# Kernel tuning notes

Hardware: AMD Instinct MI355X
Metric: run time of the kernel (lower is better)

Reference implementation:

```python
import jax, jax.numpy as jnp
import numpy as np

S, B, E, H, DFF = 1024, 4, 1024, 16, 4096
D = E // H  # head_dim = 64
EPS = 1e-5


def setup_inputs() -> dict:
    key = jax.random.key(0)
    ks = jax.random.split(key, 16)
    rn = lambda k, shape, s: jax.random.normal(k, shape, jnp.float32) * s
    # RoPE tables (half-rotation), theta=10000
    inv_freq = 1.0 / (10000.0 ** (jnp.arange(0, D, 2, dtype=jnp.float32) / D))  # [D/2]
    ang = jnp.arange(S, dtype=jnp.float32)[:, None] * inv_freq[None, :]          # [S, D/2]
    return {
        "q": rn(ks[0], (S, B, E), 1.0),
        "in_proj_w": rn(ks[1], (3 * E, E), E ** -0.5),
        "in_proj_b": rn(ks[2], (3 * E,), 0.02),
        "out_w": rn(ks[3], (E, E), E ** -0.5),
        "out_b": rn(ks[4], (E,), 0.02),
        "ln1_g": jnp.ones((E,), jnp.float32) + rn(ks[5], (E,), 0.02),
        "ln1_b": rn(ks[6], (E,), 0.02),
        "ln2_g": jnp.ones((E,), jnp.float32) + rn(ks[7], (E,), 0.02),
        "ln2_b": rn(ks[8], (E,), 0.02),
        "ff1_w": rn(ks[9], (DFF, E), E ** -0.5),
        "ff1_b": rn(ks[10], (DFF,), 0.02),
        "ff2_w": rn(ks[11], (E, DFF), DFF ** -0.5),
        "ff2_b": rn(ks[12], (E,), 0.02),
        "rope_cos": jnp.cos(ang),
        "rope_sin": jnp.sin(ang),
    }


def _layernorm(x, g, b):
    mu = jnp.mean(x, -1, keepdims=True)
    var = jnp.mean((x - mu) ** 2, -1, keepdims=True)
    return (x - mu) * jax.lax.rsqrt(var + EPS) * g + b


def reference(q, in_proj_w, in_proj_b, out_w, out_b, ln1_g, ln1_b, ln2_g, ln2_b,
              ff1_w, ff1_b, ff2_w, ff2_b, rope_cos, rope_sin):
    s, b, e = q.shape
    d = 2 * rope_cos.shape[-1]
    h = e // d
    # pre-norm (self-attention: k = v = q, so norm computed once)
    xq = _layernorm(q, ln1_g, ln1_b)
    # fused QKV projection
    qkv = xq @ in_proj_w.T + in_proj_b            # [s, b, 3e]
    qh, kh, vh = jnp.split(qkv, 3, axis=-1)
    qh = qh.reshape(s, b, h, d)
    kh = kh.reshape(s, b, h, d)
    vh = vh.reshape(s, b, h, d)

    def rope(t):
        t1, t2 = jnp.split(t, 2, axis=-1)          # [s, b, h, d/2] each
        c = rope_cos[:, None, None, :]
        sn = rope_sin[:, None, None, :]
        return jnp.concatenate([t1 * c - t2 * sn, t1 * sn + t2 * c], axis=-1)

    qh = rope(qh)
    kh = rope(kh)
    # attention (ssmax='none' -> identity scaling, dropout=0, no masks)
    scores = jnp.einsum("sbhd,tbhd->bhst", qh, kh) / jnp.sqrt(jnp.float32(d))
    attn = jax.nn.softmax(scores, axis=-1)
    ao = jnp.einsum("bhst,tbhd->sbhd", attn, vh).reshape(s, b, e)
    ao = ao @ out_w.T + out_b
    # residual + pre-norm FFN
    x = q + ao
    y = _layernorm(x, ln2_g, ln2_b)
    ff = jax.nn.gelu(y @ ff1_w.T + ff1_b, approximate=False) @ ff2_w.T + ff2_b
    return x + ff
```

## Files before the change

kernel.cpp:

```cpp
#include <hip/hip_runtime.h>
#include <hip/hip_bf16.h>
#include <stdint.h>

typedef float f32x4 __attribute__((ext_vector_type(4)));
typedef __bf16 bf16x8 __attribute__((ext_vector_type(8)));

__device__ __forceinline__ unsigned short f2bf(float f) {
    union { float f; unsigned u; } v; v.f = f;
    unsigned r = v.u + 0x7fffu + ((v.u >> 16) & 1u);
    return (unsigned short)(r >> 16);
}
__device__ __forceinline__ float bf2f(unsigned short u) {
    union { unsigned u; float f; } v; v.u = ((unsigned)u) << 16;
    return v.f;
}
__device__ __forceinline__ unsigned cvt_pk_bf16(float lo, float hi) {
    unsigned r;
    asm("v_cvt_pk_bf16_f32 %0, %1, %2" : "=v"(r) : "v"(lo), "v"(hi));
    return r;
}

__device__ __forceinline__ void gl_lds16(const void* g, void* l) {
    __builtin_amdgcn_global_load_lds(
        (const __attribute__((address_space(1))) void*)(unsigned long long)(uintptr_t)g,
        (__attribute__((address_space(3))) void*)(unsigned)(uintptr_t)l,
        16, 0, 0);
}

__global__ __launch_bounds__(256) void cvt_kernel(const float* __restrict__ in,
                                                  unsigned short* __restrict__ outp) {
    int i = blockIdx.x * 256 + threadIdx.x;
    float4 v = ((const float4*)in)[i];
    ushort4 o;
    o.x = f2bf(v.x); o.y = f2bf(v.y); o.z = f2bf(v.z); o.w = f2bf(v.w);
    ((ushort4*)outp)[i] = o;
}

__global__ __launch_bounds__(256) void ln_kernel(const float* __restrict__ x,
                                                 const float* __restrict__ g,
                                                 const float* __restrict__ b,
                                                 unsigned short* __restrict__ outp) {
    const int row = blockIdx.x;
    const int t = threadIdx.x;
    const float4 v = ((const float4*)(x + (size_t)row * 1024))[t];
    float s = v.x + v.y + v.z + v.w;
    float s2 = v.x * v.x + v.y * v.y + v.z * v.z + v.w * v.w;
    #pragma unroll
    for (int off = 1; off < 64; off <<= 1) {
        s  += __shfl_xor(s, off);
        s2 += __shfl_xor(s2, off);
    }
    __shared__ float red[8];
    const int w = t >> 6;
    if ((t & 63) == 0) { red[w * 2] = s; red[w * 2 + 1] = s2; }
    __syncthreads();
    s  = red[0] + red[2] + red[4] + red[6];
    s2 = red[1] + red[3] + red[5] + red[7];
    const float mu = s * (1.0f / 1024.0f);
    const float var = s2 * (1.0f / 1024.0f) - mu * mu;
    const float rstd = rsqrtf(var + 1e-5f);
    const float4 gv = ((const float4*)g)[t];
    const float4 bv = ((const float4*)b)[t];
    ushort4 o;
    o.x = f2bf((v.x - mu) * rstd * gv.x + bv.x);
    o.y = f2bf((v.y - mu) * rstd * gv.y + bv.y);
    o.z = f2bf((v.z - mu) * rstd * gv.z + bv.z);
    o.w = f2bf((v.w - mu) * rstd * gv.w + bv.w);
    ((ushort4*)(outp + (size_t)row * 1024))[t] = o;
}

__global__ __launch_bounds__(512) void rope_kernel(const unsigned short* __restrict__ qkv,
                                                   const float* __restrict__ rc,
                                                   const float* __restrict__ rs,
                                                   unsigned short* __restrict__ Qr,
                                                   unsigned short* __restrict__ Kr) {
    const int sb = blockIdx.x;
    const int s = sb >> 2, b = sb & 3;
    const int t = threadIdx.x;
    const int h = t >> 5, d = t & 31;
    const size_t rowo = (size_t)sb * 3072;
    const float c = rc[s * 32 + d];
    const float sn = rs[s * 32 + d];
    const size_t ho = ((size_t)(b * 16 + h) * 1024 + s) * 64;

    const float q1 = bf2f(qkv[rowo + h * 64 + d]);
    const float q2 = bf2f(qkv[rowo + h * 64 + d + 32]);
    Qr[ho + d]      = f2bf((q1 * c - q2 * sn) * 0.125f);
    Qr[ho + d + 32] = f2bf((q1 * sn + q2 * c) * 0.125f);

    const float k1 = bf2f(qkv[rowo + 1024 + h * 64 + d]);
    const float k2 = bf2f(qkv[rowo + 1024 + h * 64 + d + 32]);
    Kr[ho + d]      = f2bf(k1 * c - k2 * sn);
    Kr[ho + d + 32] = f2bf(k1 * sn + k2 * c);
}

__global__ __launch_bounds__(256) void vt_kernel(const unsigned short* __restrict__ qkv,
                                                 unsigned short* __restrict__ Vt) {
    __shared__ unsigned short t[64][66];
    const int s0 = blockIdx.x * 64;
    const int bh = blockIdx.y;
    const int b = bh >> 4, h = bh & 15;
    const int tid = threadIdx.x;
    const int si = tid >> 3, c = (tid & 7) * 8;
    #pragma unroll
    for (int r = 0; r < 2; r++) {
        const int s = si + r * 32;
        union { uint4 u; unsigned short sh[8]; } v;
        v.u = *(const uint4*)&qkv[((size_t)(s0 + s) * 4 + b) * 3072 + 2048 + h * 64 + c];
        #pragma unroll
        for (int i = 0; i < 8; i++) t[c + i][s] = v.sh[i];
    }
    __syncthreads();
    #pragma unroll
    for (int r = 0; r < 2; r++) {
        const int d = si + r * 32;
        const unsigned* rp = (const unsigned*)((const char*)&t[0][0] + d * 132 + c * 2);
        uint4 ov;
        ov.x = rp[0]; ov.y = rp[1]; ov.z = rp[2]; ov.w = rp[3];
        *(uint4*)&Vt[((size_t)bh * 64 + d) * 1024 + s0 + c] = ov;
    }
}

template <int EPI, int BM, int BN, int WM, int WN, bool CM>
__global__ __launch_bounds__((BM / WM) * (BN / WN) * 64, 2)
void gemm4(const unsigned short* __restrict__ A, const unsigned short* __restrict__ Bw,
           const float* __restrict__ bias, const float* __restrict__ res,
           void* __restrict__ Cout, int N, int K, int nbx) {
    constexpr int WAVES_N = BN / WN;
    constexpr int THREADS = (BM / WM) * (BN / WN) * 64;
    constexpr int MR = WM / 16, NR = WN / 16;
    constexpr int ASZ = BM * 64, BSZ = BN * 64;
    constexpr int RPP = THREADS / 8;
    static_assert(BM / RPP + BN / RPP == 8, "STAGE must issue exactly 8 loads");
    __shared__ __attribute__((aligned(16))) unsigned short As[2 * ASZ];
    __shared__ __attribute__((aligned(16))) unsigned short Bs[2 * BSZ];

    const int nwg = gridDim.x;
    const int swz = (blockIdx.x & 7) * (nwg >> 3) + (blockIdx.x >> 3);
    const int nby = nwg / nbx;
    const int bx = CM ? (swz / nby) : (swz % nbx);
    const int by = CM ? (swz % nby) : (swz / nbx);
    const int bm = by * BM, bn = bx * BN;

    const int tid = threadIdx.x;
    const int w = tid >> 6, l = tid & 63;
    const int wr = w / WAVES_N, wc = w % WAVES_N;
    const int lm = l & 15, lg = l >> 4, lx = lm & 7;

    const int srow = tid >> 3;
    const int sgx = ((tid & 7) ^ (srow & 7)) * 8;
    const unsigned short* Ag = A + (size_t)(bm + srow) * K + sgx;
    const unsigned short* Bg = Bw + (size_t)(bn + srow) * K + sgx;

    const int c0 = ((lg ^ lx) << 3);
    const int c1 = (((4 + lg) ^ lx) << 3);

    f32x4 acc[MR][NR];
    #pragma unroll
    for (int i = 0; i < MR; i++)
        #pragma unroll
        for (int j = 0; j < NR; j++) acc[i][j] = f32x4{0.f, 0.f, 0.f, 0.f};

    auto STAGE = [&](int buf, int k0) {
        #pragma unroll
        for (int i = 0; i < BM / RPP; i++)
            gl_lds16(Ag + (size_t)i * RPP * K + k0, &As[buf * ASZ + i * RPP * 64 + tid * 8]);
        #pragma unroll
        for (int i = 0; i < BN / RPP; i++)
            gl_lds16(Bg + (size_t)i * RPP * K + k0, &Bs[buf * BSZ + i * RPP * 64 + tid * 8]);
    };

    const int NT = K >> 6;
    STAGE(0, 0);
    STAGE(1, 64);

    int cur = 0;
    for (int t = 0; t < NT; ++t) {
        if (t + 1 < NT) asm volatile("s_waitcnt vmcnt(8)" ::: "memory");
        else            asm volatile("s_waitcnt vmcnt(0)" ::: "memory");
        __builtin_amdgcn_s_barrier();
        asm volatile("" ::: "memory");

        const int ab = cur * ASZ, bb = cur * BSZ;
        #pragma unroll
        for (int h = 0; h < 2; h++) {
            const int cc = h ? c1 : c0;
            bf16x8 af[MR], bfr[NR];
            #pragma unroll
            for (int mi = 0; mi < MR; mi++)
                af[mi] = *(const bf16x8*)&As[ab + (wr * WM + mi * 16 + lm) * 64 + cc];
            #pragma unroll
            for (int ni = 0; ni < NR; ni++)
                bfr[ni] = *(const bf16x8*)&Bs[bb + (wc * WN + ni * 16 + lm) * 64 + cc];
            __builtin_amdgcn_s_setprio(1);
            #pragma unroll
            for (int mi = 0; mi < MR; mi++)
                #pragma unroll
                for (int ni = 0; ni < NR; ni++)
                    acc[mi][ni] = __builtin_amdgcn_mfma_f32_16x16x32_bf16(
                        af[mi], bfr[ni], acc[mi][ni], 0, 0, 0);
            __builtin_amdgcn_s_setprio(0);
        }

        asm volatile("" ::: "memory");
        __builtin_amdgcn_s_barrier();
        asm volatile("" ::: "memory");
        if (t + 2 < NT) STAGE(cur, (t + 2) << 6);
        cur ^= 1;
    }

    const int r0 = bm + wr * WM + lg * 4;
    #pragma unroll
    for (int ni = 0; ni < NR; ni++) {
        const int col = bn + wc * WN + ni * 16 + lm;
        const float bc = bias[col];
        #pragma unroll
        for (int mi = 0; mi < MR; mi++) {
            #pragma unroll
            for (int j = 0; j < 4; j++) {
                const int row = r0 + mi * 16 + j;
                const size_t idx = (size_t)row * N + col;
                const float v = acc[mi][ni][j] + bc;
                if constexpr (EPI == 0) {
                    ((unsigned short*)Cout)[idx] = f2bf(v);
                } else if constexpr (EPI == 1) {
                    ((float*)Cout)[idx] = v + res[idx];
                } else if constexpr (EPI == 2) {
                    const float ge = 0.5f * v * (1.0f + erff(v * 0.70710678118654752f));
                    ((unsigned short*)Cout)[idx] = f2bf(ge);
                } else {
                    ((float*)Cout)[idx] = v + res[idx];
                }
            }
        }
    }
}

__global__ __launch_bounds__(256, 4)
void attn_kernel(const unsigned short* __restrict__ Qr, const unsigned short* __restrict__ Kr,
                 const unsigned short* __restrict__ Vt, unsigned short* __restrict__ AO) {
    __shared__ __attribute__((aligned(16))) unsigned short Ks[64][72];
    __shared__ __attribute__((aligned(16))) unsigned short Vs[64][72];
    const int tid = threadIdx.x;
    const int w = tid >> 6, l = tid & 63;
    const int lm = l & 15, lg = l >> 4;
    const int qt = blockIdx.x, bh = blockIdx.y;
    const size_t hoff = (size_t)bh * (1024 * 64);

    const size_t qrow = hoff + (size_t)(qt * 64 + w * 16 + lm) * 64;
    const bf16x8 qf0 = *(const bf16x8*)&Qr[qrow + lg * 8];
    const bf16x8 qf1 = *(const bf16x8*)&Qr[qrow + 32 + lg * 8];

    float m = -1e30f, lsum = 0.f;
    f32x4 acc[4];
    #pragma unroll
    for (int i = 0; i < 4; i++) acc[i] = f32x4{0.f, 0.f, 0.f, 0.f};

    const int sr = tid >> 3, scc = (tid & 7) * 8;
    const int srcA = lm + 16 * ((2 * lg) & 3);
    const int srcB = lm + 16 * ((2 * lg + 1) & 3);
    const bool hi2 = (lg & 2) != 0;

    uint4 kr0 = *(const uint4*)&Kr[hoff + (size_t)sr * 64 + scc];
    uint4 kr1 = *(const uint4*)&Kr[hoff + (size_t)(sr + 32) * 64 + scc];
    uint4 vr0 = *(const uint4*)&Vt[hoff + (size_t)sr * 1024 + scc];
    uint4 vr1 = *(const uint4*)&Vt[hoff + (size_t)(sr + 32) * 1024 + scc];

    for (int kt = 0; kt < 16; kt++) {
        __syncthreads();
        *(uint4*)&Ks[sr][scc]      = kr0;
        *(uint4*)&Ks[sr + 32][scc] = kr1;
        *(uint4*)&Vs[sr][scc]      = vr0;
        *(uint4*)&Vs[sr + 32][scc] = vr1;
        __syncthreads();
        if (kt < 15) {
            const size_t kb = hoff + (size_t)(kt + 1) * 64 * 64;
            kr0 = *(const uint4*)&Kr[kb + (size_t)sr * 64 + scc];
            kr1 = *(const uint4*)&Kr[kb + (size_t)(sr + 32) * 64 + scc];
            vr0 = *(const uint4*)&Vt[hoff + (size_t)sr * 1024 + (kt + 1) * 64 + scc];
            vr1 = *(const uint4*)&Vt[hoff + (size_t)(sr + 32) * 1024 + (kt + 1) * 64 + scc];
        }

        f32x4 st[4];
        #pragma unroll
        for (int nt = 0; nt < 4; nt++) {
            const bf16x8 kf0 = *(const bf16x8*)&Ks[nt * 16 + lm][lg * 8];
            const bf16x8 kf1 = *(const bf16x8*)&Ks[nt * 16 + lm][32 + lg * 8];
            f32x4 s = f32x4{0.f, 0.f, 0.f, 0.f};
            s = __builtin_amdgcn_mfma_f32_16x16x32_bf16(kf0, qf0, s, 0, 0, 0);
            s = __builtin_amdgcn_mfma_f32_16x16x32_bf16(kf1, qf1, s, 0, 0, 0);
            st[nt] = s;
        }

        float tmax = st[0][0];
        #pragma unroll
        for (int nt = 0; nt < 4; nt++)
            #pragma unroll
            for (int j = 0; j < 4; j++) tmax = fmaxf(tmax, st[nt][j]);
        tmax = fmaxf(tmax, __shfl_xor(tmax, 16));
        tmax = fmaxf(tmax, __shfl_xor(tmax, 32));

        const float mnew = fmaxf(m, tmax);
        const float fac = __builtin_amdgcn_exp2f((m - mnew) * 1.4426950408889634f);
        m = mnew;

        unsigned pd[4][2];
        float rsum = 0.f;
        #pragma unroll
        for (int nt = 0; nt < 4; nt++) {
            const float p0 = __builtin_amdgcn_exp2f((st[nt][0] - mnew) * 1.4426950408889634f);
            const float p1 = __builtin_amdgcn_exp2f((st[nt][1] - mnew) * 1.4426950408889634f);
            const float p2 = __builtin_amdgcn_exp2f((st[nt][2] - mnew) * 1.4426950408889634f);
            const float p3 = __builtin_amdgcn_exp2f((st[nt][3] - mnew) * 1.4426950408889634f);
            rsum += (p0 + p1) + (p2 + p3);
            pd[nt][0] = cvt_pk_bf16(p0, p1);
            pd[nt][1] = cvt_pk_bf16(p2, p3);
        }
        rsum += __shfl_xor(rsum, 16);
        rsum += __shfl_xor(rsum, 32);
        lsum = lsum * fac + rsum;
        #pragma unroll
        for (int nt2 = 0; nt2 < 4; nt2++)
            #pragma unroll
            for (int j = 0; j < 4; j++) acc[nt2][j] *= fac;

        #pragma unroll
        for (int kt2 = 0; kt2 < 2; kt2++) {
            const int a0 = __shfl((int)pd[kt2 * 2][0], srcA);
            const int a1 = __shfl((int)pd[kt2 * 2 + 1][0], srcA);
            const int a2 = __shfl((int)pd[kt2 * 2][1], srcA);
            const int a3 = __shfl((int)pd[kt2 * 2 + 1][1], srcA);
            const int b0 = __shfl((int)pd[kt2 * 2][0], srcB);
            const int b1 = __shfl((int)pd[kt2 * 2 + 1][0], srcB);
            const int b2 = __shfl((int)pd[kt2 * 2][1], srcB);
            const int b3 = __shfl((int)pd[kt2 * 2 + 1][1], srcB);
            union { int u[4]; bf16x8 v; } pf;
            pf.u[0] = hi2 ? a1 : a0;
            pf.u[1] = hi2 ? a3 : a2;
            pf.u[2] = hi2 ? b1 : b0;
            pf.u[3] = hi2 ? b3 : b2;
            #pragma unroll
            for (int nt2 = 0; nt2 < 4; nt2++) {
                const bf16x8 vf = *(const bf16x8*)&Vs[nt2 * 16 + lm][kt2 * 32 + lg * 8];
                acc[nt2] = __builtin_amdgcn_mfma_f32_16x16x32_bf16(vf, pf.v, acc[nt2], 0, 0, 0);
            }
        }
    }

    const int b = bh >> 4, h = bh & 15;
    const float inv = 1.0f / lsum;
    const int s = qt * 64 + w * 16 + lm;
    #pragma unroll
    for (int nt2 = 0; nt2 < 4; nt2++) {
        ushort4 o;
        o.x = f2bf(acc[nt2][0] * inv);
        o.y = f2bf(acc[nt2][1] * inv);
        o.z = f2bf(acc[nt2][2] * inv);
        o.w = f2bf(acc[nt2][3] * inv);
        *(ushort4*)&AO[(size_t)(s * 4 + b) * 1024 + h * 64 + nt2 * 16 + lg * 4] = o;
    }
}

extern "C" void kernel_launch(void* const* d_in, const int* in_sizes, int n_in,
                              void* d_out, int out_size, void* d_ws, size_t ws_size,
                              hipStream_t stream) {
    const float* q    = (const float*)d_in[0];
    const float* w_in = (const float*)d_in[1];
    const float* b_in = (const float*)d_in[2];
    const float* w_o  = (const float*)d_in[3];
    const float* b_o  = (const float*)d_in[4];
    const float* g1   = (const float*)d_in[5];
    const float* be1  = (const float*)d_in[6];
    const float* g2   = (const float*)d_in[7];
    const float* be2  = (const float*)d_in[8];
    const float* w1   = (const float*)d_in[9];
    const float* b1   = (const float*)d_in[10];
    const float* w2   = (const float*)d_in[11];
    const float* b2   = (const float*)d_in[12];
    const float* rc   = (const float*)d_in[13];
    const float* rsn  = (const float*)d_in[14];
    float* outp = (float*)d_out;

    char* base = (char*)d_ws;
    if (ws_size < 109051904ull) return;

    unsigned short* wb_in  = (unsigned short*)(base + 0);
    unsigned short* wb_out = wb_in + 3145728;
    unsigned short* wb_ff1 = wb_out + 1048576;
    unsigned short* wb_ff2 = wb_ff1 + 4194304;
    unsigned short* xq  = (unsigned short*)(base + 25165824);
    unsigned short* qkv = (unsigned short*)(base + 33554432);
    unsigned short* hh  = (unsigned short*)(base + 33554432);
    unsigned short* Qr  = (unsigned short*)(base + 58720256);
    unsigned short* Kr  = (unsigned short*)(base + 67108864);
    unsigned short* Vt  = (unsigned short*)(base + 75497472);
    unsigned short* ao  = (unsigned short*)(base + 83886080);
    float*          x   = (float*)(base + 92274688);
    unsigned short* y   = xq;

    cvt_kernel<<<3072, 256, 0, stream>>>(w_in, wb_in);
    cvt_kernel<<<1024, 256, 0, stream>>>(w_o, wb_out);
    cvt_kernel<<<4096, 256, 0, stream>>>(w1, wb_ff1);
    cvt_kernel<<<4096, 256, 0, stream>>>(w2, wb_ff2);

    ln_kernel<<<4096, 256, 0, stream>>>(q, g1, be1, xq);
    gemm4<0, 128, 128, 64, 64, false><<<768, 256, 0, stream>>>(xq, wb_in, b_in, nullptr, qkv, 3072, 1024, 24);
    rope_kernel<<<4096, 512, 0, stream>>>(qkv, rc, rsn, Qr, Kr);
    vt_kernel<<<dim3(16, 64), 256, 0, stream>>>(qkv, Vt);
    attn_kernel<<<dim3(16, 64), 256, 0, stream>>>(Qr, Kr, Vt, ao);
    gemm4<1, 128, 128, 64, 64, true><<<256, 256, 0, stream>>>(ao, wb_out, b_o, q, x, 1024, 1024, 8);
    ln_kernel<<<4096, 256, 0, stream>>>(x, g2, be2, y);
    gemm4<2, 256, 256, 128, 64, false><<<256, 512, 0, stream>>>(y, wb_ff1, b1, nullptr, hh, 4096, 1024, 16);
    gemm4<3, 128, 128, 64, 64, true><<<256, 256, 0, stream>>>(hh, wb_ff2, b2, x, outp, 1024, 4096, 8);
}
```

Before: 233.9 us.

## Add 256x256 eight-wave GEMM with interleaved prefetch for QKV and FF1

Adds a dedicated 256x256-tile GEMM kernel with 8 waves that splits each K-step into four MFMA phases. Each phase interleaves one quarter of the next tile's global-to-LDS loads and raises wave priority around the MFMA blocks. The QKV projection moves from 768 128x128 tiles to 192 256x256 tiles, and FF1 moves from the generic template to the new kernel. QKV now launches fewer blocks than the device has CUs, which risks underfilling the GPU, and the extra barriers add sync cost in exchange for better overlap.

```diff
diff --git a/kernel.cpp b/kernel.cpp
--- a/kernel.cpp
+++ b/kernel.cpp
@@ -118,6 +118,152 @@
         uint4 ov;
         ov.x = rp[0]; ov.y = rp[1]; ov.z = rp[2]; ov.w = rp[3];
         *(uint4*)&Vt[((size_t)bh * 64 + d) * 1024 + s0 + c] = ov;
+    }
+}
+
+template <int EPI>
+__global__ __launch_bounds__(512, 2)
+void gemm8(const unsigned short* __restrict__ A, const unsigned short* __restrict__ Bw,
+           const float* __restrict__ bias, const float* __restrict__ res,
+           void* __restrict__ Cout, int N, int K, int nbx) {
+    constexpr int ASZ = 256 * 64;
+    __shared__ __attribute__((aligned(16))) unsigned short As[2 * ASZ];
+    __shared__ __attribute__((aligned(16))) unsigned short Bs[2 * ASZ];
+
+    const int nwg = gridDim.x;
+    const int swz = (blockIdx.x & 7) * (nwg >> 3) + (blockIdx.x >> 3);
+    const int bx = swz % nbx, by = swz / nbx;
+    const int bm = by * 256, bn = bx * 256;
+
+    const int tid = threadIdx.x;
+    const int w = tid >> 6, l = tid & 63;
+    const int wr = w >> 2, wc = w & 3;
+    const int lm = l & 15, lg = l >> 4, lx = lm & 7;
+
+    const int srow = tid >> 3;
+    const int sgx = ((tid & 7) ^ (srow & 7)) * 8;
+    const unsigned short* Ag = A + (size_t)(bm + srow) * K + sgx;
+    const unsigned short* Bg = Bw + (size_t)(bn + srow) * K + sgx;
+
+    const int c0 = ((lg ^ lx) << 3);
+    const int c1 = (((4 + lg) ^ lx) << 3);
+
+    f32x4 acc[8][4];
+    #pragma unroll
+    for (int i = 0; i < 8; i++)
+        #pragma unroll
+        for (int j = 0; j < 4; j++) acc[i][j] = f32x4{0.f, 0.f, 0.f, 0.f};
+
+    auto SP = [&](int buf, int k0, int p) {
+        gl_lds16(Ag + (size_t)(p * 64) * K + k0, &As[buf * ASZ + p * 4096 + tid * 8]);
+        gl_lds16(Bg + (size_t)(p * 64) * K + k0, &Bs[buf * ASZ + p * 4096 + tid * 8]);
+    };
+
+    SP(0, 0, 0); SP(0, 0, 1); SP(0, 0, 2); SP(0, 0, 3);
+
+    const int NT = K >> 6;
+    const int arow = wr * 128 + lm;
+    const int brow = wc * 64 + lm;
+    int cur = 0;
+
+    for (int t = 0; t < NT; ++t) {
+        const int ab = cur * ASZ, bb = cur * ASZ;
+        const int nk0 = (t + 1) << 6;
+        const bool pf = (t + 1 < NT);
+        bf16x8 bf0[4], bf1[4], af[4];
+
+        if (pf) {
+            SP(cur ^ 1, nk0, 0);
+            asm volatile("s_waitcnt vmcnt(2)" ::: "memory");
+        } else {
+            asm volatile("s_waitcnt vmcnt(0)" ::: "memory");
+        }
+        __builtin_amdgcn_s_barrier();
+        #pragma unroll
+        for (int ni = 0; ni < 4; ni++) {
+            bf0[ni] = *(const bf16x8*)&Bs[bb + (brow + ni * 16) * 64 + c0];
+            bf1[ni] = *(const bf16x8*)&Bs[bb + (brow + ni * 16) * 64 + c1];
+        }
+        #pragma unroll
+        for (int mi = 0; mi < 4; mi++)
+            af[mi] = *(const bf16x8*)&As[ab + (arow + mi * 16) * 64 + c0];
+        __builtin_amdgcn_s_barrier();
+        __builtin_amdgcn_s_setprio(1);
+        #pragma unroll
+        for (int mi = 0; mi < 4; mi++)
+            #pragma unroll
+            for (int ni = 0; ni < 4; ni++)
+                acc[mi][ni] = __builtin_amdgcn_mfma_f32_16x16x32_bf16(af[mi], bf0[ni], acc[mi][ni], 0, 0, 0);
+        __builtin_amdgcn_s_setprio(0);
+        __builtin_amdgcn_s_barrier();
+
+        if (pf) SP(cur ^ 1, nk0, 1);
+        #pragma unroll
+        for (int mi = 0; mi < 4; mi++)
+            af[mi] = *(const bf16x8*)&As[ab + (arow + mi * 16) * 64 + c1];
+        __builtin_amdgcn_s_barrier();
+        __builtin_amdgcn_s_setprio(1);
+        #pragma unroll
+        for (int mi = 0; mi < 4; mi++)
+            #pragma unroll
+            for (int ni = 0; ni < 4; ni++)
+                acc[mi][ni] = __builtin_amdgcn_mfma_f32_16x16x32_bf16(af[mi], bf1[ni], acc[mi][ni], 0, 0, 0);
+        __builtin_amdgcn_s_setprio(0);
+        __builtin_amdgcn_s_barrier();
+
+        if (pf) SP(cur ^ 1, nk0, 2);
+        #pragma unroll
+        for (int mi = 0; mi < 4; mi++)
+            af[mi] = *(const bf16x8*)&As[ab + (arow + 64 + mi * 16) * 64 + c0];
+        __builtin_amdgcn_s_barrier();
+        __builtin_amdgcn_s_setprio(1);
+        #pragma unroll
+        for (int mi = 0; mi < 4; mi++)
+            #pragma unroll
+            for (int ni = 0; ni < 4; ni++)
+                acc[mi + 4][ni] = __builtin_amdgcn_mfma_f32_16x16x32_bf16(af[mi], bf0[ni], acc[mi + 4][ni], 0, 0, 0);
+        __builtin_amdgcn_s_setprio(0);
+        __builtin_amdgcn_s_barrier();
+
+        if (pf) SP(cur ^ 1, nk0, 3);
+        #pragma unroll
+        for (int mi = 0; mi < 4; mi++)
+            af[mi] = *(const bf16x8*)&As[ab + (arow + 64 + mi * 16) * 64 + c1];
+        __builtin_amdgcn_s_barrier();
+        __builtin_amdgcn_s_setprio(1);
+        #pragma unroll
+        for (int mi = 0; mi < 4; mi++)
+            #pragma unroll
+            for (int ni = 0; ni < 4; ni++)
+                acc[mi + 4][ni] = __builtin_amdgcn_mfma_f32_16x16x32_bf16(af[mi], bf1[ni], acc[mi + 4][ni], 0, 0, 0);
+        __builtin_amdgcn_s_setprio(0);
+        __builtin_amdgcn_s_barrier();
+
+        cur ^= 1;
+    }
+
+    const int r0 = bm + wr * 128 + lg * 4;
+    #pragma unroll
+    for (int ni = 0; ni < 4; ni++) {
+        const int col = bn + wc * 64 + ni * 16 + lm;
+        const float bc = bias[col];
+        #pragma unroll
+        for (int mi = 0; mi < 8; mi++) {
+            #pragma unroll
+            for (int j = 0; j < 4; j++) {
+                const int row = r0 + mi * 16 + j;
+                const size_t idx = (size_t)row * N + col;
+                const float v = acc[mi][ni][j] + bc;
+                if constexpr (EPI == 0) {
+                    ((unsigned short*)Cout)[idx] = f2bf(v);
+                } else if constexpr (EPI == 2) {
+                    const float ge = 0.5f * v * (1.0f + erff(v * 0.70710678118654752f));
+                    ((unsigned short*)Cout)[idx] = f2bf(ge);
+                } else {
+                    ((float*)Cout)[idx] = v + res[idx];
+                }
+            }
+        }
     }
 }
 
@@ -404,12 +550,12 @@
     cvt_kernel<<<4096, 256, 0, stream>>>(w2, wb_ff2);
 
     ln_kernel<<<4096, 256, 0, stream>>>(q, g1, be1, xq);
-    gemm4<0, 128, 128, 64, 64, false><<<768, 256, 0, stream>>>(xq, wb_in, b_in, nullptr, qkv, 3072, 1024, 24);
+    gemm8<0><<<192, 512, 0, stream>>>(xq, wb_in, b_in, nullptr, qkv, 3072, 1024, 12);
     rope_kernel<<<4096, 512, 0, stream>>>(qkv, rc, rsn, Qr, Kr);
     vt_kernel<<<dim3(16, 64), 256, 0, stream>>>(qkv, Vt);
     attn_kernel<<<dim3(16, 64), 256, 0, stream>>>(Qr, Kr, Vt, ao);
     gemm4<1, 128, 128, 64, 64, true><<<256, 256, 0, stream>>>(ao, wb_out, b_o, q, x, 1024, 1024, 8);
     ln_kernel<<<4096, 256, 0, stream>>>(x, g2, be2, y);
-    gemm4<2, 256, 256, 128, 64, false><<<256, 512, 0, stream>>>(y, wb_ff1, b1, nullptr, hh, 4096, 1024, 16);
+    gemm8<2><<<256, 512, 0, stream>>>(y, wb_ff1, b1, nullptr, hh, 4096, 1024, 16);
     gemm4<3, 128, 128, 64, 64, true><<<256, 256, 0, stream>>>(hh, wb_ff2, b2, x, outp, 1024, 4096, 8);
 }
```

After: 240.9 us. 3.0% more time.

## Add single-buffered 256x128 GEMM kernel for QKV and FF1 projections

Applied to the files above, without the earlier changes.

Introduces a new gemmW kernel with 256x128 tiles, 8 waves of 128x32 each, and a single 64 KB LDS buffer, no double buffering. It is used for the QKV and FF1 GEMMs in place of gemm4. The epilogue stages bf16 results through LDS so global stores are coalesced 16-byte writes. The intent is higher occupancy (launch bounds 512,4) and wider per-wave MFMA reuse along M. The cost is that loads no longer overlap compute within a block, which may expose memory latency, and the launch-bounds target limits registers for the 16 accumulators.

```diff
diff --git a/kernel.cpp b/kernel.cpp
--- a/kernel.cpp
+++ b/kernel.cpp
@@ -118,6 +118,99 @@
         uint4 ov;
         ov.x = rp[0]; ov.y = rp[1]; ov.z = rp[2]; ov.w = rp[3];
         *(uint4*)&Vt[((size_t)bh * 64 + d) * 1024 + s0 + c] = ov;
+    }
+}
+
+template <int EPI>
+__global__ __launch_bounds__(512, 4)
+void gemmW(const unsigned short* __restrict__ A, const unsigned short* __restrict__ Bw,
+           const float* __restrict__ bias, unsigned short* __restrict__ Cout,
+           int N, int K, int nbx) {
+    __shared__ __attribute__((aligned(16))) unsigned short smem[32768];
+    unsigned short* As = smem;
+    unsigned short* Bs = smem + 16384;
+
+    const int nwg = gridDim.x;
+    const int swz = (blockIdx.x & 7) * (nwg >> 3) + (blockIdx.x >> 3);
+    const int by = swz / nbx, bx = swz % nbx;
+    const int bm = by * 256, bn = bx * 128;
+
+    const int tid = threadIdx.x;
+    const int w = tid >> 6, l = tid & 63;
+    const int wr = w >> 2, wc = w & 3;
+    const int lm = l & 15, lg = l >> 4, lx = lm & 7;
+
+    const int srow = tid >> 3;
+    const int sgx = ((tid & 7) ^ (srow & 7)) * 8;
+    const int sdst = (tid & 7) * 8;
+    const unsigned short* Ag = A + (size_t)(bm + srow) * K + sgx;
+    const unsigned short* Bg = Bw + (size_t)(bn + srow) * K + sgx;
+
+    const int c0 = ((lg ^ lx) << 3);
+    const int c1 = (((4 + lg) ^ lx) << 3);
+
+    f32x4 acc[8][2];
+    #pragma unroll
+    for (int i = 0; i < 8; i++)
+        #pragma unroll
+        for (int j = 0; j < 2; j++) acc[i][j] = f32x4{0.f, 0.f, 0.f, 0.f};
+
+    const int arow = wr * 128 + lm;
+    const int brow = wc * 32 + lm;
+
+    for (int k0 = 0; k0 < K; k0 += 64) {
+        __syncthreads();
+        #pragma unroll
+        for (int i = 0; i < 4; i++)
+            gl_lds16(Ag + (size_t)(i * 64) * K + k0, &As[(srow + i * 64) * 64 + sdst]);
+        #pragma unroll
+        for (int i = 0; i < 2; i++)
+            gl_lds16(Bg + (size_t)(i * 64) * K + k0, &Bs[(srow + i * 64) * 64 + sdst]);
+        __syncthreads();
+        #pragma unroll
+        for (int h = 0; h < 2; h++) {
+            const int cc = h ? c1 : c0;
+            bf16x8 af[8], bfr[2];
+            #pragma unroll
+            for (int ni = 0; ni < 2; ni++)
+                bfr[ni] = *(const bf16x8*)&Bs[(brow + ni * 16) * 64 + cc];
+            #pragma unroll
+            for (int mi = 0; mi < 8; mi++)
+                af[mi] = *(const bf16x8*)&As[(arow + mi * 16) * 64 + cc];
+            #pragma unroll
+            for (int mi = 0; mi < 8; mi++)
+                #pragma unroll
+                for (int ni = 0; ni < 2; ni++)
+                    acc[mi][ni] = __builtin_amdgcn_mfma_f32_16x16x32_bf16(
+                        af[mi], bfr[ni], acc[mi][ni], 0, 0, 0);
+        }
+    }
+
+    __syncthreads();
+    const int r0l = wr * 128 + lg * 4;
+    #pragma unroll
+    for (int ni = 0; ni < 2; ni++) {
+        const int col = wc * 32 + ni * 16 + lm;
+        const float bc = bias[bn + col];
+        #pragma unroll
+        for (int mi = 0; mi < 8; mi++) {
+            #pragma unroll
+            for (int j = 0; j < 4; j++) {
+                const int row = r0l + mi * 16 + j;
+                float v = acc[mi][ni][j] + bc;
+                if constexpr (EPI == 2)
+                    v = 0.5f * v * (1.0f + erff(v * 0.70710678118654752f));
+                smem[row * 128 + col] = f2bf(v);
+            }
+        }
+    }
+    __syncthreads();
+    const int orow = tid >> 4, oseg = (tid & 15) * 8;
+    #pragma unroll
+    for (int p = 0; p < 8; p++) {
+        const int row = p * 32 + orow;
+        const uint4 v = *(const uint4*)&smem[row * 128 + oseg];
+        *(uint4*)&Cout[(size_t)(bm + row) * N + bn + oseg] = v;
     }
 }
 
@@ -404,12 +497,12 @@
     cvt_kernel<<<4096, 256, 0, stream>>>(w2, wb_ff2);
 
     ln_kernel<<<4096, 256, 0, stream>>>(q, g1, be1, xq);
-    gemm4<0, 128, 128, 64, 64, false><<<768, 256, 0, stream>>>(xq, wb_in, b_in, nullptr, qkv, 3072, 1024, 24);
+    gemmW<0><<<384, 512, 0, stream>>>(xq, wb_in, b_in, qkv, 3072, 1024, 24);
     rope_kernel<<<4096, 512, 0, stream>>>(qkv, rc, rsn, Qr, Kr);
     vt_kernel<<<dim3(16, 64), 256, 0, stream>>>(qkv, Vt);
     attn_kernel<<<dim3(16, 64), 256, 0, stream>>>(Qr, Kr, Vt, ao);
     gemm4<1, 128, 128, 64, 64, true><<<256, 256, 0, stream>>>(ao, wb_out, b_o, q, x, 1024, 1024, 8);
     ln_kernel<<<4096, 256, 0, stream>>>(x, g2, be2, y);
-    gemm4<2, 256, 256, 128, 64, false><<<256, 512, 0, stream>>>(y, wb_ff1, b1, nullptr, hh, 4096, 1024, 16);
+    gemmW<2><<<512, 512, 0, stream>>>(y, wb_ff1, b1, hh, 4096, 1024, 32);
     gemm4<3, 128, 128, 64, 64, true><<<256, 256, 0, stream>>>(hh, wb_ff2, b2, x, outp, 1024, 4096, 8);
 }
```

New measurement: 226.5 us, median of 6. -3.2%, faster.
